# Kernel optimization log

Hardware: AMD Instinct MI355X
Metric: run time of the kernel (lower is better)

## Reference

```python
import jax, jax.numpy as jnp
import numpy as np

B, T, DF, S = 64, 16, 512, 196      # batch, ticks, backbone channels, tokens
D_IN, H = 512, 8                     # attention embed dim, heads
DH = D_IN // H
DM, MEM, HN = 1024, 25, 32           # d_model neurons, memory length, NLM hidden
NSA, NSO, DOUT = 512, 512, 512       # sync sizes (random-pairing), output dim


def _ln(x, g, b, eps=1e-5):
    m = x.mean(-1, keepdims=True)
    v = ((x - m) ** 2).mean(-1, keepdims=True)
    return (x - m) / jnp.sqrt(v + eps) * g + b


def setup_inputs() -> dict:
    key = jax.random.key(0)
    ks = jax.random.split(key, 24)
    rn = lambda k, sh, sc: jax.random.normal(k, sh, jnp.float32) * sc
    p = {}
    p['x'] = rn(ks[0], (B, T, DF, S), 1.0)
    # q_proj (LazyLinear: n_sync_action -> d_input)
    p['Wqp'] = rn(ks[1], (NSA, D_IN), (1.0 / NSA) ** 0.5); p['bqp'] = jnp.zeros((D_IN,))
    # kv_proj: LazyLinear(DF->D_IN) + LayerNorm
    p['Wkv'] = rn(ks[2], (DF, D_IN), (1.0 / DF) ** 0.5); p['bkv'] = jnp.zeros((D_IN,))
    p['g_kv'] = jnp.ones((D_IN,)); p['b_kv'] = jnp.zeros((D_IN,))
    # MultiheadAttention projections
    sc = (1.0 / D_IN) ** 0.5
    p['Wq'] = rn(ks[3], (D_IN, D_IN), sc); p['bq'] = jnp.zeros((D_IN,))
    p['Wk'] = rn(ks[4], (D_IN, D_IN), sc); p['bk'] = jnp.zeros((D_IN,))
    p['Wv'] = rn(ks[5], (D_IN, D_IN), sc); p['bv'] = jnp.zeros((D_IN,))
    p['Wo'] = rn(ks[6], (D_IN, D_IN), sc); p['bo'] = jnp.zeros((D_IN,))
    # synapses: Linear(D_IN+DM -> 2*DM) + GLU + LayerNorm(DM)
    p['Wsyn'] = rn(ks[7], (D_IN + DM, 2 * DM), (1.0 / (D_IN + DM)) ** 0.5)
    p['bsyn'] = jnp.zeros((2 * DM,))
    p['g_syn'] = jnp.ones((DM,)); p['b_syn'] = jnp.zeros((DM,))
    # NLM: per-neuron 2-layer MLP over memory window
    p['W1'] = rn(ks[8], (DM, MEM, HN), (1.0 / MEM) ** 0.5); p['b1'] = jnp.zeros((DM, HN))
    p['W2'] = rn(ks[9], (DM, HN), (1.0 / HN) ** 0.5); p['b2'] = jnp.zeros((DM,))
    # learned initial states
    p['init_act'] = rn(ks[10], (DM,), (1.0 / DM) ** 0.5)
    p['init_hist'] = rn(ks[11], (DM, MEM), (1.0 / (DM + MEM)) ** 0.5)
    # decay params (init zero in torch)
    p['decay_a'] = jnp.zeros((NSA,)); p['decay_o'] = jnp.zeros((NSO,))
    # output projection (LazyLinear: n_sync_out -> d_output)
    p['Wout'] = rn(ks[12], (NSO, DOUT), (1.0 / NSO) ** 0.5); p['bout'] = jnp.zeros((DOUT,))
    # random-pairing neuron indices (buffers, constants)
    p['li_a'] = jax.random.randint(ks[13], (NSA,), 0, DM, jnp.int32)
    p['ri_a'] = jax.random.randint(ks[14], (NSA,), 0, DM, jnp.int32)
    p['li_o'] = jax.random.randint(ks[15], (NSO,), 0, DM, jnp.int32)
    p['ri_o'] = jax.random.randint(ks[16], (NSO,), 0, DM, jnp.int32)
    return p


def reference(x, Wqp, bqp, Wkv, bkv, g_kv, b_kv, Wq, bq, Wk, bk, Wv, bv, Wo, bo,
              Wsyn, bsyn, g_syn, b_syn, W1, b1, W2, b2, init_act, init_hist,
              decay_a, decay_o, Wout, bout, li_a, ri_a, li_o, ri_o):
    r_a = jnp.exp(-jnp.clip(decay_a, 0.0, 15.0))   # [NSA]
    r_o = jnp.exp(-jnp.clip(decay_o, 0.0, 15.0))   # [NSO]
    act0 = jnp.broadcast_to(init_act, (B, DM))
    hist0 = jnp.broadcast_to(init_hist, (B, DM, MEM))
    # initial 'out' sync state (decay_alpha=pairwise, decay_beta=ones)
    ao0 = act0[:, li_o] * act0[:, ri_o]
    bo0 = jnp.ones_like(ao0)
    # 'action' state starts None -> zeros so first update gives alpha=pairwise, beta=1
    aa0 = jnp.zeros((B, NSA), x.dtype); ba0 = jnp.zeros((B, NSA), x.dtype)

    def mha(q, kv):
        # q [B,1,D_IN], kv [B,S,D_IN]
        qh = (q @ Wq + bq).reshape(B, 1, H, DH)
        kh = (kv @ Wk + bk).reshape(B, S, H, DH)
        vh = (kv @ Wv + bv).reshape(B, S, H, DH)
        sc = jnp.einsum('bqhd,bkhd->bhqk', qh, kh) / jnp.sqrt(jnp.float32(DH))
        a = jax.nn.softmax(sc, axis=-1)
        o = jnp.einsum('bhqk,bkhd->bqhd', a, vh).reshape(B, 1, D_IN)
        return o @ Wo + bo

    def tick(carry, xt):
        act, hist, aa, ba, ao, bo_ = carry
        # compute_kv: identity backbone, flatten(2).transpose(1,2) -> [B,S,DF]
        kv = _ln(jnp.swapaxes(xt, 1, 2) @ Wkv + bkv, g_kv, b_kv)
        # action sync
        aa = r_a * aa + act[:, li_a] * act[:, ri_a]
        ba = r_a * ba + 1.0
        sync_a = aa / jnp.sqrt(ba)
        q = (sync_a @ Wqp + bqp)[:, None, :]
        attn = mha(q, kv)[:, 0]                         # [B,D_IN]
        pre = jnp.concatenate([attn, act], axis=-1)     # [B,D_IN+DM]
        g = pre @ Wsyn + bsyn
        a_, b_ = jnp.split(g, 2, axis=-1)
        pre_act = _ln(a_ * jax.nn.sigmoid(b_), g_syn, b_syn)  # [B,DM]
        hist = jnp.concatenate([hist[:, :, 1:], pre_act[:, :, None]], axis=2)
        # NLM: per-neuron MLP over memory window
        h = jax.nn.relu(jnp.einsum('bnm,nmh->bnh', hist, W1) + b1)
        act = jnp.einsum('bnh,nh->bn', h, W2) + b2
        # out sync
        ao = r_o * ao + act[:, li_o] * act[:, ri_o]
        bo_ = r_o * bo_ + 1.0
        sync_o = ao / jnp.sqrt(bo_)
        pred = sync_o @ Wout + bout                      # [B,DOUT]
        logp = jax.nn.log_softmax(pred, axis=-1)
        ne = -(jnp.exp(logp) * logp).sum(-1) / jnp.log(jnp.float32(DOUT))
        cert = jnp.stack([ne, 1.0 - ne], axis=-1)        # [B,2]
        return (act, hist, aa, ba, ao, bo_), (pred, cert)

    xt = jnp.moveaxis(x, 1, 0)  # [T,B,DF,S]
    _, (preds, certs) = jax.lax.scan(tick, (act0, hist0, aa0, ba0, ao0, bo0), xt)
    predictions = jnp.moveaxis(preds, 0, -1)   # [B,DOUT,T]
    certainties = jnp.moveaxis(certs, 0, -1)   # [B,2,T]
    return predictions, certainties
```

## Files before the change

### kernel.cpp

```cpp
#include <hip/hip_runtime.h>
#include <stdint.h>
#include <stddef.h>

#define B_    64
#define T_    16
#define DF_   512
#define S_    196
#define DIN_  512
#define H_    8
#define DH_   64
#define DM_   1024
#define MEM_  25
#define HN_   32
#define MR_   (B_*S_)
#define TC_   2
#define NCH_  (T_/TC_)
#define MCC_  (MR_*TC_)

typedef short bf16x8 __attribute__((ext_vector_type(8)));
typedef short short4v __attribute__((ext_vector_type(4)));
typedef float f32x4  __attribute__((ext_vector_type(4)));

__device__ __forceinline__ float b2f(short h){
  unsigned u = ((unsigned)(unsigned short)h) << 16;
// ... 194 lines not shown
      __syncthreads();
      short* dst = xT + (size_t)((t0n2 + ti)*B_ + b) * S_ * DIN_;
      #pragma unroll
      for (int i = 0; i < 4; ++i) {
        int s  = s0 + ty + i*8;
        int df = df0 + tx;
        if (s < S_) dst[(size_t)s*DF_ + df] = f2b(tile[tx*33 + ty+i*8]);
      }
      __syncthreads();
    }
  } else if (op == 1) {
    int twin = tid >> 8;
    short* lA = (short*)pool;
    short* lB = (short*)(pool + 16384 + 16384*twin);
    int p = idx; if (p > 391) p = 391;
    int bx = p % 196, byp = p / 196;
    const short* xTn = xT + (size_t)t0n1 * MR_ * 512;
    gemm_body<0,0>(tid & 255, bx, byp*2 + twin, twin == 0, lA, lB,
                   xTn, WkvT, kvpN, bkv, bkv, 1 << 30,
                   nullptr, nullptr, nullptr, nullptr,
                   McN, 512, 512, 512, 512);
  } else if (op == 2) {
    int blk = idx;
    int w = tid >> 6, l = tid & 63;
    for (int i = 0; i < 8; ++i) {
      int r = blk*64 + i*8 + w;
      if (r < McN) {
        bf16x8 v8 = *(const bf16x8*)&kvpN[(size_t)r*512 + l*8];
        float s = 0.f, s2 = 0.f;
        #pragma unroll
        for (int j = 0; j < 8; ++j) { float v = b2f(v8[j]); s += v; s2 += v*v; }
        #pragma unroll
        for (int m = 1; m < 64; m <<= 1) { s += __shfl_xor(s, m, 64); s2 += __shfl_xor(s2, m, 64); }
        if (l == 0) {
          float mean = s * (1.f/512.f);
          float var  = s2 * (1.f/512.f) - mean*mean;
          muN[r] = mean;
          ivN[r] = rsqrtf(var + 1e-5f);
        }
      }
    }
  } else if (op == 3) {
    int twin = tid >> 8;
    short* lA = (short*)pool;
    short* lB = (short*)(pool + 16384 + 16384*twin);
    int p = idx; if (p > 783) p = 783;
    int bx = p % 8, byp = p / 8;
    gemm_body<0,2>(tid & 255, bx, byp*2 + twin, twin == 0, lA, lB,
                   WkkvT, kvpN, KVTN, nullptr, nullptr, 0,
                   muN, ivN, gw, bw, 1024, McN, 512, 512, McN);
  }
}

__device__ __forceinline__ void attn_body(int b, int tid, float* smem,
    const float* actT, float* aa, float* ba,
    const int* li_a, const int* ri_a, const float* decay_a,
    const short* WqqB, const float* bqh,
    const short* KVT, int ldkv, int ti, short* preb)
{
  float* syncL = smem;
  float* qhL   = smem + 512;
  float* pL    = smem + 1024;
  int j = tid;
  float rr = expf(-clip015(decay_a[j]));
  float prod = actT[li_a[j]*64 + b] * actT[ri_a[j]*64 + b];
  float a2 = rr*aa[b*512+j] + prod; aa[b*512+j] = a2;
  float bb2 = rr*ba[b*512+j] + 1.f;  ba[b*512+j] = bb2;
  syncL[j] = a2 * rsqrtf(bb2);
  __syncthreads();
  float qa = bqh[j];
  #pragma unroll 8
  for (int k = 0; k < 512; ++k) qa += syncL[k]*b2f(WqqB[k*512+j]);
  qhL[j] = qa;
  __syncthreads();
  int h = tid >> 6, l = tid & 63;
  const size_t cb = (size_t)(ti*B_ + b) * S_;
  const short* Kb = KVT + (size_t)(h*64)*ldkv + cb;
  int s3 = 192 + l; int s3c = s3 < S_ ? s3 : S_-1;
  float sc0=0.f, sc1=0.f, sc2=0.f, sc3=0.f;
  #pragma unroll 8
  for (int d = 0; d < 64; ++d) {
    const short* kr = Kb + (size_t)d*ldkv;
    float qv = qhL[h*64 + d];
    sc0 += qv * b2f(kr[l]);
    sc1 += qv * b2f(kr[64 + l]);
    sc2 += qv * b2f(kr[128 + l]);
    sc3 += qv * b2f(kr[s3c]);
  }
  sc0 *= 0.125f; sc1 *= 0.125f; sc2 *= 0.125f;
  sc3 = (s3 < S_) ? sc3*0.125f : -1e30f;
  float mx = fmaxf(fmaxf(sc0, sc1), fmaxf(sc2, sc3));
  #pragma unroll
  for (int k = 32; k >= 1; k >>= 1) mx = fmaxf(mx, __shfl_xor(mx, k, 64));
  float p0 = expf(sc0-mx), p1 = expf(sc1-mx), p2 = expf(sc2-mx), p3 = expf(sc3-mx);
  pL[h*256 + l] = p0; pL[h*256 + 64+l] = p1;
  pL[h*256 + 128+l] = p2; pL[h*256 + 192+l] = p3;
  float ps = p0+p1+p2+p3;
  #pragma unroll
  for (int k = 32; k >= 1; k >>= 1) ps += __shfl_xor(ps, k, 64);
  float inv = 1.f / ps;
  __syncthreads();
  const short4v* vrow = (const short4v*)(KVT + (size_t)(512 + h*64 + l)*ldkv + cb);
  const float* pp = pL + h*256;
  float ac0=0.f, ac1=0.f, ac2=0.f, ac3=0.f;
  #pragma unroll 7
  for (int c = 0; c < 49; ++c) {
    short4v v4 = vrow[c];
    ac0 += pp[c*4]   * b2f(v4.x);
    ac1 += pp[c*4+1] * b2f(v4.y);
    ac2 += pp[c*4+2] * b2f(v4.z);
    ac3 += pp[c*4+3] * b2f(v4.w);
  }
  float accv = (ac0+ac1)+(ac2+ac3);
  preb[(size_t)b*1536 + h*64 + l] = f2b(accv * inv);
}

__device__ __forceinline__ void outk_body(int tt, int b, int tid,
    float* syncL, float* wred,
    const float* actT, float* ao, float* bo_s,
    const int* li_o, const int* ri_o, const float* decay_o,
    const short* WoutB, const float* bout, float* out)
{
  int j = tid;
  float rr = expf(-clip015(decay_o[j]));
  float prod = actT[li_o[j]*64 + b] * actT[ri_o[j]*64 + b];
  float a2 = rr*ao[b*512+j] + prod; ao[b*512+j] = a2;
  float bb2 = rr*bo_s[b*512+j] + 1.f; bo_s[b*512+j] = bb2;
  syncL[j] = a2 * rsqrtf(bb2);
  __syncthreads();
  float a = bout[j];
  #pragma unroll 8
  for (int k = 0; k < 512; ++k) a += syncL[k]*b2f(WoutB[k*512+j]);
  out[((size_t)b*512 + j)*16 + tt] = a;
  int w = tid >> 6, l = tid & 63;
  float m = a;
  #pragma unroll
  for (int k = 32; k >= 1; k >>= 1) m = fmaxf(m, __shfl_xor(m, k, 64));
  if (l == 0) wred[w] = m;
  __syncthreads();
  float M = wred[0];
  #pragma unroll
  for (int k = 1; k < 8; ++k) M = fmaxf(M, wred[k]);
  float e = expf(a - M);
  float z = e, s1 = e*(a - M);
  #pragma unroll
  for (int k = 32; k >= 1; k >>= 1) { z += __shfl_xor(z, k, 64); s1 += __shfl_xor(s1, k, 64); }
  if (l == 0) { wred[8+w] = z; wred[16+w] = s1; }
  __syncthreads();
  if (tid == 0) {
    float Z = 0.f, S1 = 0.f;
    #pragma unroll
    for (int k = 0; k < 8; ++k) { Z += wred[8+k]; S1 += wred[16+k]; }
    float plp = S1 / Z - logf(Z);
    float ne = -plp * (1.f/logf(512.f));
    out[524288 + (size_t)b*32 + tt]      = ne;
    out[524288 + (size_t)b*32 + 16 + tt] = 1.f - ne;
  }
}

__device__ __forceinline__ void synglu_body(int bid, int tid, char* pool,
    const short* preb, const short* WsynP, const float* bsynF, float* u)
{
  f32x4* part = (f32x4*)pool;
  int w = tid >> 6, l = tid & 63;
  int mf = w & 3, kh = w >> 2;
  int arow = mf*16 + (l & 15);
  int kbase = kh*768 + (l >> 4)*8;
  const short* ap = preb + (size_t)arow*1536 + kbase;
  const short* bp = WsynP + (size_t)(bid*16 + (l & 15))*1536 + kbase;
  f32x4 acc = (f32x4){0.f,0.f,0.f,0.f};
  #pragma unroll 4
  for (int ks = 0; ks < 24; ++ks) {
    bf16x8 av = *(const bf16x8*)(ap + ks*32);
    bf16x8 bv = *(const bf16x8*)(bp + ks*32);
    acc = __builtin_amdgcn_mfma_f32_16x16x32_bf16(av, bv, acc, 0, 0, 0);
  }
  part[w*64 + l] = acc;
  __syncthreads();
  if (w < 4) {
    f32x4 o1 = part[w*64 + l], o2 = part[(w+4)*64 + l];
    int c = l & 15;
    int colg = bid*8 + (c & 7);
    float bias = (c < 8) ? bsynF[colg] : bsynF[1024 + colg];
    float tv[4], pv[4];
    #pragma unroll
    for (int r2 = 0; r2 < 4; ++r2) tv[r2] = o1[r2] + o2[r2] + bias;
    #pragma unroll
    for (int r2 = 0; r2 < 4; ++r2) pv[r2] = __shfl_xor(tv[r2], 8, 64);
    if (c < 8) {
      #pragma unroll
      for (int r2 = 0; r2 < 4; ++r2) {
        float uu = tv[r2] * (1.f/(1.f + expf(-pv[r2])));
        int brow = w*16 + (l >> 4)*4 + r2;
        u[brow*1024 + colg] = uu;
      }
    }
  }
}

__device__ __forceinline__ void nlmln_body(int bid, int tid, char* pool,
    const float* u, const float* gsyn, const float* bln, float* hist,
    const float* W1, const float* b1, const float* W2, const float* b2,
    float* actT, short* preb, int t)
{
  float* mstat = (float*)pool;
  float* istat = mstat + 64;
  {
    int b = tid >> 3, p = tid & 7;
    const float* up = u + b*1024 + p*128;
    float s = 0.f, s2 = 0.f;
    #pragma unroll 8
    for (int i = 0; i < 128; ++i) { float v = up[i]; s += v; s2 += v*v; }
    #pragma unroll
    for (int k = 4; k >= 1; k >>= 1) { s += __shfl_xor(s, k, 64); s2 += __shfl_xor(s2, k, 64); }
    if (p == 0) {
      float mean = s * (1.f/1024.f);
      float var  = s2 * (1.f/1024.f) - mean*mean;
      mstat[b] = mean;
      istat[b] = rsqrtf(var + 1e-5f);
    }
  }
  __syncthreads();
  int n = (bid << 3) + (tid >> 6), b = tid & 63;
  float nv = (u[b*1024 + n] - mstat[b]) * istat[b] * gsyn[n] + bln[n];
  int slot = t % MEM_;
  hist[((size_t)n*MEM_ + slot)*64 + b] = nv;
  float h[32];
  #pragma unroll
  for (int j = 0; j < 32; ++j) h[j] = b1[n*32+j];
  #pragma unroll 5
  for (int m = 0; m < MEM_; ++m) {
    int phys = (t + 1 + m) % MEM_;
    float hv = (m == MEM_-1) ? nv : hist[((size_t)n*MEM_ + phys)*64 + b];
    const float* wp = &W1[((size_t)n*MEM_ + m)*32];
    #pragma unroll
    for (int j = 0; j < 32; ++j) h[j] += hv * wp[j];
  }
  float acc = b2[n];
  #pragma unroll
  for (int j = 0; j < 32; ++j) acc += fmaxf(h[j], 0.f) * W2[n*32+j];
  actT[n*64 + b] = acc;
  preb[(size_t)b*1536 + 512 + n] = f2b(acc);
}

#define PIGGY_ARGS int opA, int pfA, int nA, int opB, int pfB, \
    const float* __restrict__ xg, int t0n1, int t0n2, short* __restrict__ xTg, \
    const short* __restrict__ WkvT, \
    const float* __restrict__ bkv, short* __restrict__ kvpN, \
    float* __restrict__ muN, float* __restrict__ ivN, \
    const short* __restrict__ WkkvT, const float* __restrict__ gw, \
    const float* __restrict__ bw, short* __restrict__ KVTN, int McN
#define PIGGY_CALL do { \
    int pb = (int)blockIdx.x - 128; \
    int op_, idx_; \
    if (pb < nA) { op_ = opA; idx_ = pfA + pb; } \
    else         { op_ = opB; idx_ = pfB + (pb - nA); } \
    run_piggy(tid, op_, idx_, pool, xg, t0n1, t0n2, xTg, WkvT, bkv, \
              kvpN, muN, ivN, WkkvT, gw, bw, KVTN, McN); \
  } while (0)

__global__ __launch_bounds__(512) void stageA(
    const float* __restrict__ actT,
    float* __restrict__ aa, float* __restrict__ ba,
    const int* __restrict__ li_a, const int* __restrict__ ri_a,
    const float* __restrict__ decay_a,
    const short* __restrict__ WqqB, const float* __restrict__ bqh,
    const short* __restrict__ KVT, int ldkv, int ti,
    short* __restrict__ preb,
    float* __restrict__ ao, float* __restrict__ bo_s,
    const int* __restrict__ li_o, const int* __restrict__ ri_o,
    const float* __restrict__ decay_o,
    const short* __restrict__ WoutB, const float* __restrict__ bout,
    float* __restrict__ out, int t, PIGGY_ARGS)
{
  __shared__ __attribute__((aligned(16))) char pool[49152];
  const int bid = blockIdx.x, tid = threadIdx.x;
  if (bid < 128) {
    float* smem = (float*)pool;
    if (bid < 64)
      attn_body(bid, tid, smem, actT, aa, ba, li_a, ri_a, decay_a,
                WqqB, bqh, KVT, ldkv, ti, preb);
    else if (t > 0)
      outk_body(t-1, bid-64, tid, smem, smem+512, actT, ao, bo_s,
                li_o, ri_o, decay_o, WoutB, bout, out);
  } else {
    PIGGY_CALL;
  }
}

__global__ __launch_bounds__(512) void stageB(
    const short* __restrict__ preb, const short* __restrict__ WsynP,
    const float* __restrict__ bsynF, float* __restrict__ u, PIGGY_ARGS)
{
  __shared__ __attribute__((aligned(16))) char pool[49152];
  const int bid = blockIdx.x, tid = threadIdx.x;
  if (bid < 128) synglu_body(bid, tid, pool, preb, WsynP, bsynF, u);
  else PIGGY_CALL;
}

__global__ __launch_bounds__(512) void stageC(
    const float* __restrict__ u, const float* __restrict__ gsyn,
    const float* __restrict__ bln, float* __restrict__ hist,
    const float* __restrict__ W1, const float* __restrict__ b1,
    const float* __restrict__ W2, const float* __restrict__ b2,
    float* __restrict__ actT, short* __restrict__ preb, int t, PIGGY_ARGS)
{
  __shared__ __attribute__((aligned(16))) char pool[49152];
  const int bid = blockIdx.x, tid = threadIdx.x;
  if (bid < 128) nlmln_body(bid, tid, pool, u, gsyn, bln, hist,
                            W1, b1, W2, b2, actT, preb, t);
  else PIGGY_CALL;
}

__global__ __launch_bounds__(512) void outk_fin(
    const float* __restrict__ actT,
    float* __restrict__ ao, float* __restrict__ bo_s,
    const int* __restrict__ li_o, const int* __restrict__ ri_o,
    const float* __restrict__ decay_o,
    const short* __restrict__ WoutB, const float* __restrict__ bout,
    float* __restrict__ out)
{
  __shared__ __attribute__((aligned(16))) float smem[544];
  outk_body(T_-1, blockIdx.x, threadIdx.x, smem, smem+512, actT, ao, bo_s,
            li_o, ri_o, decay_o, WoutB, bout, out);
}

__global__ __launch_bounds__(256) void xpose_x(const float* __restrict__ x,
                                               short* __restrict__ xT, int t0, int tc)
{
  __shared__ float tile[32][33];
  int df0 = blockIdx.x*32, s0 = blockIdx.y*32;
  int z = blockIdx.z;
  int b = z / tc, ti = z % tc;
  int tx = threadIdx.x & 31, ty = threadIdx.x >> 5;
  const float* src = x + (size_t)(b*T_ + t0 + ti) * DF_ * S_;
  #pragma unroll
  for (int i = 0; i < 4; ++i) {
    int df = df0 + ty + i*8;
    int s  = s0 + tx;
    tile[ty+i*8][tx] = (s < S_) ? src[(size_t)df*S_ + s] : 0.f;
  }
  __syncthreads();
  short* dst = xT + (size_t)((t0 + ti)*B_ + b) * S_ * DIN_;
  #pragma unroll
  for (int i = 0; i < 4; ++i) {
    int s  = s0 + ty + i*8;
    int df = df0 + tx;
    if (s < S_) dst[(size_t)s*DF_ + df] = f2b(tile[tx][ty+i*8]);
  }
}

__global__ __launch_bounds__(256) void ln_stats(const short* __restrict__ in,
    float* __restrict__ mu, float* __restrict__ iv, int nrows)
{
  int w = threadIdx.x >> 6, l = threadIdx.x & 63;
  int r = blockIdx.x*4 + w;
  if (r >= nrows) return;
  bf16x8 v8 = *(const bf16x8*)&in[(size_t)r*512 + l*8];
  float s = 0.f, s2 = 0.f;
  #pragma unroll
  for (int j = 0; j < 8; ++j) { float v = b2f(v8[j]); s += v; s2 += v*v; }
  #pragma unroll
  for (int m = 1; m < 64; m <<= 1) { s += __shfl_xor(s, m, 64); s2 += __shfl_xor(s2, m, 64); }
  if (l == 0) {
    float mean = s * (1.f/512.f);
    float var  = s2 * (1.f/512.f) - mean*mean;
    mu[r] = mean;
    iv[r] = rsqrtf(var + 1e-5f);
  }
}

__global__ __launch_bounds__(256) void prep_all(
    const float* __restrict__ Wkv, const float* __restrict__ Wk,
    const float* __restrict__ Wv,  const float* __restrict__ Wsyn,
    const float* __restrict__ Wq,  const float* __restrict__ Wqp,
    const float* __restrict__ Wo,  const float* __restrict__ Wout,
    const float* __restrict__ g_kv, const float* __restrict__ b_kv,
    const float* __restrict__ bk, const float* __restrict__ bv,
    const float* __restrict__ bqp, const float* __restrict__ bq,
    const float* __restrict__ bo_p, const float* __restrict__ bsyn,
    short* __restrict__ WkvT, short* __restrict__ WkkvT,
    short* __restrict__ WsynF, short* __restrict__ WsynTt,
    short* __restrict__ WqT, short* __restrict__ WqpB,
    short* __restrict__ WoB, short* __restrict__ WoutB,
    float* __restrict__ bqh, float* __restrict__ bsynF,
    float* __restrict__ gw, float* __restrict__ bw,
    float* __restrict__ aa, float* __restrict__ ba,
    float* __restrict__ ao, float* __restrict__ bo_s,
    float* __restrict__ actT, float* __restrict__ hist,
    short* __restrict__ preb,
    const float* __restrict__ init_act, const float* __restrict__ init_hist,
    const int* __restrict__ li_o, const int* __restrict__ ri_o,
    const float* __restrict__ x, short* __restrict__ xT)
{
  __shared__ float tile[32][33];
  const int blk = blockIdx.x, tid = threadIdx.x;
  auto wtr = [&](const float* in, short* out, int bx, int by,
                 int C, int ldo, int coff, const float* scale){
    int c0 = bx*32, r0 = by*32;
    int tx = tid & 31, ty = tid >> 5;
    #pragma unroll
    for (int i = 0; i < 4; ++i) {
      int r = r0+ty+i*8;
      float sc = scale ? scale[r] : 1.f;
      tile[ty+i*8][tx] = in[(size_t)r*C + c0+tx] * sc;
    }
    __syncthreads();
    #pragma unroll
    for (int i = 0; i < 4; ++i)
      out[(size_t)(c0+ty+i*8)*ldo + coff + r0+tx] = f2b(tile[tx][ty+i*8]);
  };
  auto cvt4 = [&](const float* in, short* out, int sb){
    int i = (sb*256 + tid)*4;
    #pragma unroll
    for (int j = 0; j < 4; ++j) out[i+j] = f2b(in[i+j]);
  };
  auto bfold = [&](const float* vec, const float* W, const float* base,
                   float* out, int n, int ldw){
    float a = base ? base[n] : 0.f;
    #pragma unroll 8
    for (int k = 0; k < 512; ++k) a += vec[k]*W[(size_t)k*ldw + n];
    out[n] = a;
  };

  if (blk < 256)       wtr(Wkv, WkvT, blk & 15, blk >> 4, 512, 512, 0, nullptr);
  else if (blk < 512)  { int s = blk-256;  wtr(Wk, WkkvT, s & 15, s >> 4, 512, 512, 0, g_kv); }
  else if (blk < 768)  { int s = blk-512;  wtr(Wv, WkkvT + (size_t)512*512, s & 15, s >> 4, 512, 512, 0, g_kv); }
  else if (blk < 2816) { int s = blk-768;  wtr(Wsyn + (size_t)512*2048, WsynF, s % 64, s / 64, 2048, 1536, 512, nullptr); }
  else if (blk < 3840) { int s = blk-2816; wtr(Wsyn, WsynTt, s % 64, s / 64, 2048, 512, 0, nullptr); }
  else if (blk < 4096) { int s = blk-3840; wtr(Wq, WqT, s & 15, s >> 4, 512, 512, 0, nullptr); }
  else if (blk < 4352) cvt4(Wqp,  WqpB,  blk-4096);
  else if (blk < 4608) cvt4(Wo,   WoB,   blk-4352);
  else if (blk < 4864) cvt4(Wout, WoutB, blk-4608);
  else if (blk < 4882) {
    int j = blk-4864;
    if (j < 2)        bfold(bqp,  Wq,   bq,   bqh,   j*256 + tid,      512);
    else if (j < 10)  bfold(bo_p, Wsyn, bsyn, bsynF, (j-2)*256 + tid,  2048);
    else if (j < 12)  bfold(g_kv, Wk,   nullptr, gw,       (j-10)*256 + tid, 512);
    else if (j < 14)  bfold(g_kv, Wv,   nullptr, gw + 512, (j-12)*256 + tid, 512);
    else if (j < 16)  bfold(b_kv, Wk,   bk,   bw,       (j-14)*256 + tid, 512);
    else              bfold(b_kv, Wv,   bv,   bw + 512, (j-16)*256 + tid, 512);
  } else if (blk < 11282) {
    int i = (blk-4882)*256 + tid;
    if (i < 64*512) {
      aa[i] = 0.f; ba[i] = 0.f;
      int j = i & 511;
      ao[i] = init_act[li_o[j]] * init_act[ri_o[j]];
      bo_s[i] = 1.f;
    }
    if (i < 65536) {
      int n = i >> 6, b = i & 63;
      actT[i] = init_act[n];
      preb[(size_t)b*1536 + 512 + n] = f2b(init_act[n]);
    }
    if (i < DM_*MEM_*64) {
      int nm = i >> 6;
      hist[i] = init_hist[nm];
    }
  } else {
    int tx = tid & 31, ty = tid >> 5;
    int base = (blk - 11282) * 16;
    for (int it = 0; it < 16; ++it) {
      int gt = base + it;
      int df0 = (gt & 15) * 32;
      int r = gt >> 4;
      int s0 = (r % 7) * 32;
      int z = r / 7;
      int b = z >> 2, t = z & 3;
      const float* src = x + (size_t)(b*T_ + t) * DF_ * S_;
      #pragma unroll
      for (int i = 0; i < 4; ++i) {
        int df = df0 + ty + i*8;
        int s  = s0 + tx;
        tile[ty+i*8][tx] = (s < S_) ? src[(size_t)df*S_ + s] : 0.f;
      }
      __syncthreads();
      short* dst = xT + (size_t)(t*B_ + b) * S_ * DIN_;
      #pragma unroll
      for (int i = 0; i < 4; ++i) {
        int s  = s0 + ty + i*8;
        int df = df0 + tx;
        if (s < S_) dst[(size_t)s*DF_ + df] = f2b(tile[tx][ty+i*8]);
      }
      __syncthreads();
    }
  }
}

extern "C" void kernel_launch(void* const* d_in, const int* in_sizes, int n_in,
                              void* d_out, int out_size, void* d_ws, size_t ws_size,
                              hipStream_t stream)
{
  (void)in_sizes; (void)n_in; (void)out_size;
  const float* x       = (const float*)d_in[0];
  const float* Wqp     = (const float*)d_in[1];
  const float* bqp     = (const float*)d_in[2];
  const float* Wkv     = (const float*)d_in[3];
  const float* bkv     = (const float*)d_in[4];
  const float* g_kv    = (const float*)d_in[5];
  const float* b_kv    = (const float*)d_in[6];
  const float* Wq      = (const float*)d_in[7];
  const float* bq      = (const float*)d_in[8];
  const float* Wk      = (const float*)d_in[9];
  const float* bk      = (const float*)d_in[10];
  const float* Wv      = (const float*)d_in[11];
  const float* bv      = (const float*)d_in[12];
  const float* Wo      = (const float*)d_in[13];
  const float* bo_p    = (const float*)d_in[14];
  const float* Wsyn    = (const float*)d_in[15];
  const float* bsyn    = (const float*)d_in[16];
  const float* g_syn   = (const float*)d_in[17];
  const float* b_syn   = (const float*)d_in[18];
  const float* W1      = (const float*)d_in[19];
  const float* b1      = (const float*)d_in[20];
  const float* W2      = (const float*)d_in[21];
  const float* b2      = (const float*)d_in[22];
  const float* init_act  = (const float*)d_in[23];
  const float* init_hist = (const float*)d_in[24];
  const float* decay_a = (const float*)d_in[25];
  const float* decay_o = (const float*)d_in[26];
  const float* Wout    = (const float*)d_in[27];
  const float* bout    = (const float*)d_in[28];
  const int* li_a = (const int*)d_in[29];
  const int* ri_a = (const int*)d_in[30];
  const int* li_o = (const int*)d_in[31];
  const int* ri_o = (const int*)d_in[32];

  char* ws = (char*)d_ws;
  size_t off = 0;
  auto alloc = [&](size_t bytes) { char* p = ws + off; off += (bytes + 255) & ~(size_t)255; return p; };
  short* WkvT   = (short*)alloc(512*512*2);
  short* WkkvT  = (short*)alloc(1024*512*2);
  short* WsynF  = (short*)alloc(2048*1536*2);
  short* WsynP  = (short*)alloc(2048*1536*2);
  short* WsynTt = (short*)alloc(2048*512*2);
  short* WqpB   = (short*)alloc(512*512*2);
  short* WqT    = (short*)alloc(512*512*2);
  short* WoB    = (short*)alloc(512*512*2);
  short* WqqB   = (short*)alloc(512*512*2);
  short* WoutB  = (short*)alloc(512*512*2);
  float* bqh    = (float*)alloc(512*4);
  float* bsynF  = (float*)alloc(2048*4);
  float* gw     = (float*)alloc(1024*4);
  float* bw     = (float*)alloc(1024*4);
  short* preb   = (short*)alloc(64*1536*2);
  float* u      = (float*)alloc(64*1024*4);
  float* aa     = (float*)alloc(64*512*4);
  float* ba     = (float*)alloc(64*512*4);
  float* ao     = (float*)alloc(64*512*4);
  float* bo_s   = (float*)alloc(64*512*4);
  float* actT   = (float*)alloc(1024*64*4);
  float* hist   = (float*)alloc((size_t)1024*25*64*4);
  size_t fixed_end = off;

  const size_t szXT  = (size_t)T_*MR_*512*2;
  const size_t szKVP = (size_t)MCC_*512*2;
  const size_t szKVT = (size_t)MCC_*1024*2;
  const size_t szST  = (size_t)MCC_*4;
  size_t need_full = fixed_end + szXT + 2*szKVP + 2*szKVT + 4*szST + 4096;
  bool pig_en = (ws_size >= need_full);

  short* xT = (short*)alloc(szXT);
  short* kvpB[2]; short* KVTB[2]; float* muB[2]; float* ivB[2];
  kvpB[0] = (short*)alloc(szKVP);
  KVTB[0] = (short*)alloc(szKVT);
  muB[0]  = (float*)alloc(szST);
  ivB[0]  = (float*)alloc(szST);
  if (pig_en) {
    kvpB[1] = (short*)alloc(szKVP);
    KVTB[1] = (short*)alloc(szKVT);
    muB[1]  = (float*)alloc(szST);
    ivB[1]  = (float*)alloc(szST);
  } else {
    kvpB[1] = kvpB[0]; KVTB[1] = KVTB[0]; muB[1] = muB[0]; ivB[1] = ivB[0];
  }

  const int BIG = 1 << 30;
  const float* FN = nullptr;

  prep_all<<<13074, 256, 0, stream>>>(Wkv, Wk, Wv, Wsyn, Wq, Wqp, Wo, Wout,
      g_kv, b_kv, bk, bv, bqp, bq, bo_p, bsyn,
      WkvT, WkkvT, WsynF, WsynTt, WqT, WqpB, WoB, WoutB,
      bqh, bsynF, gw, bw, aa, ba, ao, bo_s, actT, hist, preb,
      init_act, init_hist, li_o, ri_o, x, xT);
  if (!pig_en)
    xpose_x<<<dim3(16,7,B_*(T_-2*TC_)), 256, 0, stream>>>(x, xT, 2*TC_, T_-2*TC_);
  gemm_prep3<<<864, 256, 0, stream>>>(WqpB, WqT, WqqB, WsynTt, WoB, WsynF,
                                      xT, WkvT, bkv, kvpB[0]);
  permstats<<<2048 + MCC_/4, 256, 0, stream>>>(WsynF, WsynP, kvpB[0], muB[0], ivB[0]);
  gemm_k<0,2><<<dim3(8,196), 256, 0, stream>>>(WkkvT, kvpB[0], KVTB[0], nullptr, nullptr, BIG,
                                               muB[0], ivB[0], gw, bw, 1024, MCC_, 512, 512, MCC_);

  auto run_pipe = [&](int c, short* kvpP, float* muP, float* ivP, short* KVTP){
    const short* xTc = xT + (size_t)c*TC_*MR_*512;
    gemm_k<0,0><<<dim3(196,4), 256, 0, stream>>>(xTc, WkvT, kvpP, bkv, bkv, BIG,
                                                 FN, FN, FN, FN, MCC_, 512, 512, 512, 512);
    ln_stats<<<MCC_/4, 256, 0, stream>>>(kvpP, muP, ivP, MCC_);
    gemm_k<0,2><<<dim3(8,196), 256, 0, stream>>>(WkkvT, kvpP, KVTP, nullptr, nullptr, BIG,
                                                 muP, ivP, gw, bw, 1024, MCC_, 512, 512, MCC_);
  };

  auto pigcfg = [](int q, bool p123, bool p4,
                   int& opA, int& pfA, int& nA, int& opB, int& pfB, int& nB){
    opA = 0; pfA = 0; nA = 0; opB = 0; pfB = 0; nB = 0;
    if (q == 0 || q == 1) {
      if (p123) { opA = 1; pfA = q*196; nA = 196; }
      if (p4)   { opB = 4; pfB = q*224; nB = 224; }
    } else if (q == 2) {
      if (p123) { opA = 2; pfA = 0; nA = 392; }
    } else {
      if (p123) { opA = 3; pfA = (q-3)*262; nA = (q == 5) ? 260 : 262; }
    }
  };

  for (int c = 0; c < NCH_; ++c) {
    int par = pig_en ? (c & 1) : 0;
    int nxt = pig_en ? (par ^ 1) : 0;
    if (!pig_en && c > 0) run_pipe(c, kvpB[0], muB[0], ivB[0], KVTB[0]);
    bool p123 = pig_en && (c < NCH_-1);
    bool p4   = pig_en && (c < NCH_-2);
    int t0n1 = (c < NCH_-1) ? (c+1)*TC_ : 0;
    int t0n2 = (c < NCH_-2) ? (c+2)*TC_ : 0;
    for (int ti = 0; ti < TC_; ++ti) {
      int t = c*TC_ + ti;
      int oA, fA, nA, oB, fB, nB;
      pigcfg(ti*3+0, p123, p4, oA, fA, nA, oB, fB, nB);
      stageA<<<128+nA+nB, 512, 0, stream>>>(actT, aa, ba, li_a, ri_a, decay_a,
          WqqB, bqh, KVTB[par], MCC_, ti, preb,
          ao, bo_s, li_o, ri_o, decay_o, WoutB, bout, (float*)d_out, t,
          oA, fA, nA, oB, fB, x, t0n1, t0n2, xT, WkvT, bkv,
          kvpB[nxt], muB[nxt], ivB[nxt], WkkvT, gw, bw, KVTB[nxt], MCC_);
      pigcfg(ti*3+1, p123, p4, oA, fA, nA, oB, fB, nB);
      stageB<<<128+nA+nB, 512, 0, stream>>>(preb, WsynP, bsynF, u,
          oA, fA, nA, oB, fB, x, t0n1, t0n2, xT, WkvT, bkv,
          kvpB[nxt], muB[nxt], ivB[nxt], WkkvT, gw, bw, KVTB[nxt], MCC_);
      pigcfg(ti*3+2, p123, p4, oA, fA, nA, oB, fB, nB);
      stageC<<<128+nA+nB, 512, 0, stream>>>(u, g_syn, b_syn, hist,
          W1, b1, W2, b2, actT, preb, t,
          oA, fA, nA, oB, fB, x, t0n1, t0n2, xT, WkvT, bkv,
          kvpB[nxt], muB[nxt], ivB[nxt], WkkvT, gw, bw, KVTB[nxt], MCC_);
    }
  }
  outk_fin<<<64, 512, 0, stream>>>(actT, ao, bo_s, li_o, ri_o, decay_o,
                                   WoutB, bout, (float*)d_out);
}
```

Before: 2.046 ms.

## Fuse NLM/LayerNorm, output sync and attention into one per-batch stage kernel

Merges the per-tick stageC (LayerNorm + NLM), the output-sync head and stageA (action sync + attention) into a single stageCA kernel where each of 64 blocks handles one batch row. The block keeps activations in shared memory, which removes one launch per tick and the global actT round trip. The history buffer is relaid out batch-major so each block owns its own slice, and the piggybacked KV-precompute work is redistributed across two launches instead of three. In exchange, this phase now uses only 64 blocks that each do the full 1024-neuron NLM serially with two neurons per thread, which reduces parallelism on the critical path.

```diff
diff --git a/kernel.cpp b/kernel.cpp
--- a/kernel.cpp
+++ b/kernel.cpp
@@ -270,197 +270,6 @@
   }
 }
 
-__device__ __forceinline__ void attn_body(int b, int tid, float* smem,
-    const float* actT, float* aa, float* ba,
-    const int* li_a, const int* ri_a, const float* decay_a,
-    const short* WqqB, const float* bqh,
-    const short* KVT, int ldkv, int ti, short* preb)
-{
-  float* syncL = smem;
-  float* qhL   = smem + 512;
-  float* pL    = smem + 1024;
-  int j = tid;
-  float rr = expf(-clip015(decay_a[j]));
-  float prod = actT[li_a[j]*64 + b] * actT[ri_a[j]*64 + b];
-  float a2 = rr*aa[b*512+j] + prod; aa[b*512+j] = a2;
-  float bb2 = rr*ba[b*512+j] + 1.f;  ba[b*512+j] = bb2;
-  syncL[j] = a2 * rsqrtf(bb2);
-  __syncthreads();
-  float qa = bqh[j];
-  #pragma unroll 8
-  for (int k = 0; k < 512; ++k) qa += syncL[k]*b2f(WqqB[k*512+j]);
-  qhL[j] = qa;
-  __syncthreads();
-  int h = tid >> 6, l = tid & 63;
-  const size_t cb = (size_t)(ti*B_ + b) * S_;
-  const short* Kb = KVT + (size_t)(h*64)*ldkv + cb;
-  int s3 = 192 + l; int s3c = s3 < S_ ? s3 : S_-1;
-  float sc0=0.f, sc1=0.f, sc2=0.f, sc3=0.f;
-  #pragma unroll 8
-  for (int d = 0; d < 64; ++d) {
-    const short* kr = Kb + (size_t)d*ldkv;
-    float qv = qhL[h*64 + d];
-    sc0 += qv * b2f(kr[l]);
-    sc1 += qv * b2f(kr[64 + l]);
-    sc2 += qv * b2f(kr[128 + l]);
-    sc3 += qv * b2f(kr[s3c]);
-  }
-  sc0 *= 0.125f; sc1 *= 0.125f; sc2 *= 0.125f;
-  sc3 = (s3 < S_) ? sc3*0.125f : -1e30f;
-  float mx = fmaxf(fmaxf(sc0, sc1), fmaxf(sc2, sc3));
-  #pragma unroll
-  for (int k = 32; k >= 1; k >>= 1) mx = fmaxf(mx, __shfl_xor(mx, k, 64));
-  float p0 = expf(sc0-mx), p1 = expf(sc1-mx), p2 = expf(sc2-mx), p3 = expf(sc3-mx);
-  pL[h*256 + l] = p0; pL[h*256 + 64+l] = p1;
-  pL[h*256 + 128+l] = p2; pL[h*256 + 192+l] = p3;
-  float ps = p0+p1+p2+p3;
-  #pragma unroll
-  for (int k = 32; k >= 1; k >>= 1) ps += __shfl_xor(ps, k, 64);
-  float inv = 1.f / ps;
-  __syncthreads();
-  const short4v* vrow = (const short4v*)(KVT + (size_t)(512 + h*64 + l)*ldkv + cb);
-  const float* pp = pL + h*256;
-  float ac0=0.f, ac1=0.f, ac2=0.f, ac3=0.f;
-  #pragma unroll 7
-  for (int c = 0; c < 49; ++c) {
-    short4v v4 = vrow[c];
-    ac0 += pp[c*4]   * b2f(v4.x);
-    ac1 += pp[c*4+1] * b2f(v4.y);
-    ac2 += pp[c*4+2] * b2f(v4.z);
-    ac3 += pp[c*4+3] * b2f(v4.w);
-  }
-  float accv = (ac0+ac1)+(ac2+ac3);
-  preb[(size_t)b*1536 + h*64 + l] = f2b(accv * inv);
-}
-
-__device__ __forceinline__ void outk_body(int tt, int b, int tid,
-    float* syncL, float* wred,
-    const float* actT, float* ao, float* bo_s,
-    const int* li_o, const int* ri_o, const float* decay_o,
-    const short* WoutB, const float* bout, float* out)
-{
-  int j = tid;
-  float rr = expf(-clip015(decay_o[j]));
-  float prod = actT[li_o[j]*64 + b] * actT[ri_o[j]*64 + b];
-  float a2 = rr*ao[b*512+j] + prod; ao[b*512+j] = a2;
-  float bb2 = rr*bo_s[b*512+j] + 1.f; bo_s[b*512+j] = bb2;
-  syncL[j] = a2 * rsqrtf(bb2);
-  __syncthreads();
-  float a = bout[j];
-  #pragma unroll 8
-  for (int k = 0; k < 512; ++k) a += syncL[k]*b2f(WoutB[k*512+j]);
-  out[((size_t)b*512 + j)*16 + tt] = a;
-  int w = tid >> 6, l = tid & 63;
-  float m = a;
-  #pragma unroll
-  for (int k = 32; k >= 1; k >>= 1) m = fmaxf(m, __shfl_xor(m, k, 64));
-  if (l == 0) wred[w] = m;
-  __syncthreads();
-  float M = wred[0];
-  #pragma unroll
-  for (int k = 1; k < 8; ++k) M = fmaxf(M, wred[k]);
-  float e = expf(a - M);
-  float z = e, s1 = e*(a - M);
-  #pragma unroll
-  for (int k = 32; k >= 1; k >>= 1) { z += __shfl_xor(z, k, 64); s1 += __shfl_xor(s1, k, 64); }
-  if (l == 0) { wred[8+w] = z; wred[16+w] = s1; }
-  __syncthreads();
-  if (tid == 0) {
-    float Z = 0.f, S1 = 0.f;
-    #pragma unroll
-    for (int k = 0; k < 8; ++k) { Z += wred[8+k]; S1 += wred[16+k]; }
-    float plp = S1 / Z - logf(Z);
-    float ne = -plp * (1.f/logf(512.f));
-    out[524288 + (size_t)b*32 + tt]      = ne;
-    out[524288 + (size_t)b*32 + 16 + tt] = 1.f - ne;
-  }
-}
-
-__device__ __forceinline__ void synglu_body(int bid, int tid, char* pool,
-    const short* preb, const short* WsynP, const float* bsynF, float* u)
-{
-  f32x4* part = (f32x4*)pool;
-  int w = tid >> 6, l = tid & 63;
-  int mf = w & 3, kh = w >> 2;
-  int arow = mf*16 + (l & 15);
-  int kbase = kh*768 + (l >> 4)*8;
-  const short* ap = preb + (size_t)arow*1536 + kbase;
-  const short* bp = WsynP + (size_t)(bid*16 + (l & 15))*1536 + kbase;
-  f32x4 acc = (f32x4){0.f,0.f,0.f,0.f};
-  #pragma unroll 4
-  for (int ks = 0; ks < 24; ++ks) {
-    bf16x8 av = *(const bf16x8*)(ap + ks*32);
-    bf16x8 bv = *(const bf16x8*)(bp + ks*32);
-    acc = __builtin_amdgcn_mfma_f32_16x16x32_bf16(av, bv, acc, 0, 0, 0);
-  }
-  part[w*64 + l] = acc;
-  __syncthreads();
-  if (w < 4) {
-    f32x4 o1 = part[w*64 + l], o2 = part[(w+4)*64 + l];
-    int c = l & 15;
-    int colg = bid*8 + (c & 7);
-    float bias = (c < 8) ? bsynF[colg] : bsynF[1024 + colg];
-    float tv[4], pv[4];
-    #pragma unroll
-    for (int r2 = 0; r2 < 4; ++r2) tv[r2] = o1[r2] + o2[r2] + bias;
-    #pragma unroll
-    for (int r2 = 0; r2 < 4; ++r2) pv[r2] = __shfl_xor(tv[r2], 8, 64);
-    if (c < 8) {
-      #pragma unroll
-      for (int r2 = 0; r2 < 4; ++r2) {
-        float uu = tv[r2] * (1.f/(1.f + expf(-pv[r2])));
-        int brow = w*16 + (l >> 4)*4 + r2;
-        u[brow*1024 + colg] = uu;
-      }
-    }
-  }
-}
-
-__device__ __forceinline__ void nlmln_body(int bid, int tid, char* pool,
-    const float* u, const float* gsyn, const float* bln, float* hist,
-    const float* W1, const float* b1, const float* W2, const float* b2,
-    float* actT, short* preb, int t)
-{
-  float* mstat = (float*)pool;
-  float* istat = mstat + 64;
-  {
-    int b = tid >> 3, p = tid & 7;
-    const float* up = u + b*1024 + p*128;
-    float s = 0.f, s2 = 0.f;
-    #pragma unroll 8
-    for (int i = 0; i < 128; ++i) { float v = up[i]; s += v; s2 += v*v; }
-    #pragma unroll
-    for (int k = 4; k >= 1; k >>= 1) { s += __shfl_xor(s, k, 64); s2 += __shfl_xor(s2, k, 64); }
-    if (p == 0) {
-      float mean = s * (1.f/1024.f);
-      float var  = s2 * (1.f/1024.f) - mean*mean;
-      mstat[b] = mean;
-      istat[b] = rsqrtf(var + 1e-5f);
-    }
-  }
-  __syncthreads();
-  int n = (bid << 3) + (tid >> 6), b = tid & 63;
-  float nv = (u[b*1024 + n] - mstat[b]) * istat[b] * gsyn[n] + bln[n];
-  int slot = t % MEM_;
-  hist[((size_t)n*MEM_ + slot)*64 + b] = nv;
-  float h[32];
-  #pragma unroll
-  for (int j = 0; j < 32; ++j) h[j] = b1[n*32+j];
-  #pragma unroll 5
-  for (int m = 0; m < MEM_; ++m) {
-    int phys = (t + 1 + m) % MEM_;
-    float hv = (m == MEM_-1) ? nv : hist[((size_t)n*MEM_ + phys)*64 + b];
-    const float* wp = &W1[((size_t)n*MEM_ + m)*32];
-    #pragma unroll
-    for (int j = 0; j < 32; ++j) h[j] += hv * wp[j];
-  }
-  float acc = b2[n];
-  #pragma unroll
-  for (int j = 0; j < 32; ++j) acc += fmaxf(h[j], 0.f) * W2[n*32+j];
-  actT[n*64 + b] = acc;
-  preb[(size_t)b*1536 + 512 + n] = f2b(acc);
-}
-
 #define PIGGY_ARGS int opA, int pfA, int nA, int opB, int pfB, \
     const float* __restrict__ xg, int t0n1, int t0n2, short* __restrict__ xTg, \
     const short* __restrict__ WkvT, \
@@ -468,8 +277,8 @@
     float* __restrict__ muN, float* __restrict__ ivN, \
     const short* __restrict__ WkkvT, const float* __restrict__ gw, \
     const float* __restrict__ bw, short* __restrict__ KVTN, int McN
-#define PIGGY_CALL do { \
-    int pb = (int)blockIdx.x - 128; \
+#define PIGGY_BODY(BASE) do { \
+    int pb = (int)blockIdx.x - (BASE); \
     int op_, idx_; \
     if (pb < nA) { op_ = opA; idx_ = pfA + pb; } \
     else         { op_ = opB; idx_ = pfB + (pb - nA); } \
@@ -477,8 +286,13 @@
               kvpN, muN, ivN, WkkvT, gw, bw, KVTN, McN); \
   } while (0)
 
-__global__ __launch_bounds__(512) void stageA(
-    const float* __restrict__ actT,
+__global__ __launch_bounds__(512) void stageCA(
+    const float* __restrict__ u,
+    const float* __restrict__ gsyn, const float* __restrict__ bln,
+    float* __restrict__ histB,
+    const float* __restrict__ W1, const float* __restrict__ b1,
+    const float* __restrict__ W2, const float* __restrict__ b2,
+    const float* __restrict__ init_act,
     float* __restrict__ aa, float* __restrict__ ba,
     const int* __restrict__ li_a, const int* __restrict__ ri_a,
     const float* __restrict__ decay_a,
@@ -489,58 +303,222 @@
     const int* __restrict__ li_o, const int* __restrict__ ri_o,
     const float* __restrict__ decay_o,
     const short* __restrict__ WoutB, const float* __restrict__ bout,
-    float* __restrict__ out, int t, PIGGY_ARGS)
+    float* __restrict__ out, int t, int dopre, int doattn, PIGGY_ARGS)
+{
+  __shared__ __attribute__((aligned(16))) char pool[49152];
+  const int bid = blockIdx.x, tid = threadIdx.x;
+  if (bid < 64) {
+    const int b = bid;
+    float* actL  = (float*)pool;
+    float* syncL = actL + 1024;
+    float* wred  = syncL + 512;
+    float* qhL   = wred + 32;
+    float* pL    = qhL + 512;
+    int w = tid >> 6, l = tid & 63;
+    if (dopre) {
+      const int tp = t - 1;
+      const int slot = tp % MEM_;
+      float v0 = u[b*1024 + tid], v1 = u[b*1024 + 512 + tid];
+      float s = v0 + v1, s2 = v0*v0 + v1*v1;
+      #pragma unroll
+      for (int k = 32; k >= 1; k >>= 1) { s += __shfl_xor(s, k, 64); s2 += __shfl_xor(s2, k, 64); }
+      if (l == 0) { wred[w] = s; wred[8+w] = s2; }
+      __syncthreads();
+      float S = 0.f, S2 = 0.f;
+      #pragma unroll
+      for (int k = 0; k < 8; ++k) { S += wred[k]; S2 += wred[8+k]; }
+      float mean = S * (1.f/1024.f);
+      float var  = S2 * (1.f/1024.f) - mean*mean;
+      float inv  = rsqrtf(var + 1e-5f);
+      float nv0 = (v0 - mean)*inv*gsyn[tid]     + bln[tid];
+      float nv1 = (v1 - mean)*inv*gsyn[tid+512] + bln[tid+512];
+      float h[32];
+      {
+        const int n = tid;
+        float* hb = histB + ((size_t)b*1024 + n)*MEM_;
+        #pragma unroll
+        for (int j = 0; j < 32; ++j) h[j] = b1[n*32+j];
+        #pragma unroll 5
+        for (int m = 0; m < MEM_; ++m) {
+          int phys = (tp + 1 + m) % MEM_;
+          float hv = (m == MEM_-1) ? nv0 : hb[phys];
+          const float* wp = &W1[((size_t)n*MEM_ + m)*32];
+          #pragma unroll
+          for (int j = 0; j < 32; ++j) h[j] += hv * wp[j];
+        }
+        hb[slot] = nv0;
+        float acc = b2[n];
+        #pragma unroll
+        for (int j = 0; j < 32; ++j) acc += fmaxf(h[j], 0.f) * W2[n*32+j];
+        actL[n] = acc;
+        preb[(size_t)b*1536 + 512 + n] = f2b(acc);
+      }
+      {
+        const int n = tid + 512;
+        float* hb = histB + ((size_t)b*1024 + n)*MEM_;
+        #pragma unroll
+        for (int j = 0; j < 32; ++j) h[j] = b1[n*32+j];
+        #pragma unroll 5
+        for (int m = 0; m < MEM_; ++m) {
+          int phys = (tp + 1 + m) % MEM_;
+          float hv = (m == MEM_-1) ? nv1 : hb[phys];
+          const float* wp = &W1[((size_t)n*MEM_ + m)*32];
+          #pragma unroll
+          for (int j = 0; j < 32; ++j) h[j] += hv * wp[j];
+        }
+        hb[slot] = nv1;
+        float acc = b2[n];
+        #pragma unroll
+        for (int j = 0; j < 32; ++j) acc += fmaxf(h[j], 0.f) * W2[n*32+j];
+        actL[n] = acc;
+        preb[(size_t)b*1536 + 512 + n] = f2b(acc);
+      }
+      __syncthreads();
+      {
+        int j = tid;
+        float rr = expf(-clip015(decay_o[j]));
+        float prod = actL[li_o[j]] * actL[ri_o[j]];
+        float a2 = rr*ao[b*512+j] + prod; ao[b*512+j] = a2;
+        float bb2 = rr*bo_s[b*512+j] + 1.f; bo_s[b*512+j] = bb2;
+        syncL[j] = a2 * rsqrtf(bb2);
+        __syncthreads();
+        float a = bout[j];
+        #pragma unroll 8
+        for (int k = 0; k < 512; ++k) a += syncL[k]*b2f(WoutB[k*512+j]);
+        out[((size_t)b*512 + j)*16 + tp] = a;
+        float m = a;
+        #pragma unroll
+        for (int k = 32; k >= 1; k >>= 1) m = fmaxf(m, __shfl_xor(m, k, 64));
+        if (l == 0) wred[w] = m;
+        __syncthreads();
+        float M = wred[0];
+        #pragma unroll
+        for (int k = 1; k < 8; ++k) M = fmaxf(M, wred[k]);
+        float e = expf(a - M);
+        float z = e, s1 = e*(a - M);
+        #pragma unroll
+        for (int k = 32; k >= 1; k >>= 1) { z += __shfl_xor(z, k, 64); s1 += __shfl_xor(s1, k, 64); }
+        if (l == 0) { wred[8+w] = z; wred[16+w] = s1; }
+        __syncthreads();
+        if (tid == 0) {
+          float Z = 0.f, S1 = 0.f;
+          #pragma unroll
+          for (int k = 0; k < 8; ++k) { Z += wred[8+k]; S1 += wred[16+k]; }
+          float plp = S1 / Z - logf(Z);
+          float ne = -plp * (1.f/logf(512.f));
+          out[524288 + (size_t)b*32 + tp]      = ne;
+          out[524288 + (size_t)b*32 + 16 + tp] = 1.f - ne;
+        }
+      }
+    } else {
+      actL[tid]       = init_act[tid];
+      actL[tid + 512] = init_act[tid + 512];
+    }
+    __syncthreads();
+    if (doattn) {
+      int j = tid;
+      float rr = expf(-clip015(decay_a[j]));
+      float prod = actL[li_a[j]] * actL[ri_a[j]];
+      float a2 = rr*aa[b*512+j] + prod; aa[b*512+j] = a2;
+      float bb2 = rr*ba[b*512+j] + 1.f;  ba[b*512+j] = bb2;
+      syncL[j] = a2 * rsqrtf(bb2);
+      __syncthreads();
+      float qa = bqh[j];
+      #pragma unroll 8
+      for (int k = 0; k < 512; ++k) qa += syncL[k]*b2f(WqqB[k*512+j]);
+      qhL[j] = qa;
+      __syncthreads();
+      int h8 = tid >> 6;
+      const size_t cb = (size_t)(ti*B_ + b) * S_;
+      const short* Kb = KVT + (size_t)(h8*64)*ldkv + cb;
+      int s3 = 192 + l; int s3c = s3 < S_ ? s3 : S_-1;
+      float sc0=0.f, sc1=0.f, sc2=0.f, sc3=0.f;
+      #pragma unroll 8
+      for (int d = 0; d < 64; ++d) {
+        const short* kr = Kb + (size_t)d*ldkv;
+        float qv = qhL[h8*64 + d];
+        sc0 += qv * b2f(kr[l]);
+        sc1 += qv * b2f(kr[64 + l]);
+        sc2 += qv * b2f(kr[128 + l]);
+        sc3 += qv * b2f(kr[s3c]);
+      }
+      sc0 *= 0.125f; sc1 *= 0.125f; sc2 *= 0.125f;
+      sc3 = (s3 < S_) ? sc3*0.125f : -1e30f;
+      float mx = fmaxf(fmaxf(sc0, sc1), fmaxf(sc2, sc3));
+      #pragma unroll
+      for (int k = 32; k >= 1; k >>= 1) mx = fmaxf(mx, __shfl_xor(mx, k, 64));
+      float p0 = expf(sc0-mx), p1 = expf(sc1-mx), p2 = expf(sc2-mx), p3 = expf(sc3-mx);
+      pL[h8*256 + l] = p0; pL[h8*256 + 64+l] = p1;
+      pL[h8*256 + 128+l] = p2; pL[h8*256 + 192+l] = p3;
+      float ps = p0+p1+p2+p3;
+      #pragma unroll
+      for (int k = 32; k >= 1; k >>= 1) ps += __shfl_xor(ps, k, 64);
+      float inv2 = 1.f / ps;
+      __syncthreads();
+      const short4v* vrow = (const short4v*)(KVT + (size_t)(512 + h8*64 + l)*ldkv + cb);
+      const float* pp = pL + h8*256;
+      float ac0=0.f, ac1=0.f, ac2=0.f, ac3=0.f;
+      #pragma unroll 7
+      for (int c = 0; c < 49; ++c) {
+        short4v v4 = vrow[c];
+        ac0 += pp[c*4]   * b2f(v4.x);
+        ac1 += pp[c*4+1] * b2f(v4.y);
+        ac2 += pp[c*4+2] * b2f(v4.z);
+        ac3 += pp[c*4+3] * b2f(v4.w);
+      }
+      float accv = (ac0+ac1)+(ac2+ac3);
+      preb[(size_t)b*1536 + h8*64 + l] = f2b(accv * inv2);
+    }
+  } else {
+    PIGGY_BODY(64);
+  }
+}
+
+__global__ __launch_bounds__(512) void stageB(
+    const short* __restrict__ preb, const short* __restrict__ WsynP,
+    const float* __restrict__ bsynF, float* __restrict__ u, PIGGY_ARGS)
 {
   __shared__ __attribute__((aligned(16))) char pool[49152];
   const int bid = blockIdx.x, tid = threadIdx.x;
   if (bid < 128) {
-    float* smem = (float*)pool;
-    if (bid < 64)
-      attn_body(bid, tid, smem, actT, aa, ba, li_a, ri_a, decay_a,
-                WqqB, bqh, KVT, ldkv, ti, preb);
-    else if (t > 0)
-      outk_body(t-1, bid-64, tid, smem, smem+512, actT, ao, bo_s,
-                li_o, ri_o, decay_o, WoutB, bout, out);
+    f32x4* part = (f32x4*)pool;
+    int w = tid >> 6, l = tid & 63;
+    int mf = w & 3, kh = w >> 2;
+    int arow = mf*16 + (l & 15);
+    int kbase = kh*768 + (l >> 4)*8;
+    const short* ap = preb + (size_t)arow*1536 + kbase;
+    const short* bp = WsynP + (size_t)(bid*16 + (l & 15))*1536 + kbase;
+    f32x4 acc = (f32x4){0.f,0.f,0.f,0.f};
+    #pragma unroll 4
+    for (int ks = 0; ks < 24; ++ks) {
+      bf16x8 av = *(const bf16x8*)(ap + ks*32);
+      bf16x8 bv = *(const bf16x8*)(bp + ks*32);
+      acc = __builtin_amdgcn_mfma_f32_16x16x32_bf16(av, bv, acc, 0, 0, 0);
+    }
+    part[w*64 + l] = acc;
+    __syncthreads();
+    if (w < 4) {
+      f32x4 o1 = part[w*64 + l], o2 = part[(w+4)*64 + l];
+      int c = l & 15;
+      int colg = bid*8 + (c & 7);
+      float bias = (c < 8) ? bsynF[colg] : bsynF[1024 + colg];
+      float tv[4], pv[4];
+      #pragma unroll
+      for (int r2 = 0; r2 < 4; ++r2) tv[r2] = o1[r2] + o2[r2] + bias;
+      #pragma unroll
+      for (int r2 = 0; r2 < 4; ++r2) pv[r2] = __shfl_xor(tv[r2], 8, 64);
+      if (c < 8) {
+        #pragma unroll
+        for (int r2 = 0; r2 < 4; ++r2) {
+          float uu = tv[r2] * (1.f/(1.f + expf(-pv[r2])));
+          int brow = w*16 + (l >> 4)*4 + r2;
+          u[brow*1024 + colg] = uu;
+        }
+      }
+    }
   } else {
-    PIGGY_CALL;
-  }
-}
-
-__global__ __launch_bounds__(512) void stageB(
-    const short* __restrict__ preb, const short* __restrict__ WsynP,
-    const float* __restrict__ bsynF, float* __restrict__ u, PIGGY_ARGS)
-{
-  __shared__ __attribute__((aligned(16))) char pool[49152];
-  const int bid = blockIdx.x, tid = threadIdx.x;
-  if (bid < 128) synglu_body(bid, tid, pool, preb, WsynP, bsynF, u);
-  else PIGGY_CALL;
-}
-
-__global__ __launch_bounds__(512) void stageC(
-    const float* __restrict__ u, const float* __restrict__ gsyn,
-    const float* __restrict__ bln, float* __restrict__ hist,
-    const float* __restrict__ W1, const float* __restrict__ b1,
-    const float* __restrict__ W2, const float* __restrict__ b2,
-    float* __restrict__ actT, short* __restrict__ preb, int t, PIGGY_ARGS)
-{
-  __shared__ __attribute__((aligned(16))) char pool[49152];
-  const int bid = blockIdx.x, tid = threadIdx.x;
-  if (bid < 128) nlmln_body(bid, tid, pool, u, gsyn, bln, hist,
-                            W1, b1, W2, b2, actT, preb, t);
-  else PIGGY_CALL;
-}
-
-__global__ __launch_bounds__(512) void outk_fin(
-    const float* __restrict__ actT,
-    float* __restrict__ ao, float* __restrict__ bo_s,
-    const int* __restrict__ li_o, const int* __restrict__ ri_o,
-    const float* __restrict__ decay_o,
-    const short* __restrict__ WoutB, const float* __restrict__ bout,
-    float* __restrict__ out)
-{
-  __shared__ __attribute__((aligned(16))) float smem[544];
-  outk_body(T_-1, blockIdx.x, threadIdx.x, smem, smem+512, actT, ao, bo_s,
-            li_o, ri_o, decay_o, WoutB, bout, out);
+    PIGGY_BODY(128);
+  }
 }
 
 __global__ __launch_bounds__(256) void xpose_x(const float* __restrict__ x,
@@ -605,8 +583,7 @@
     float* __restrict__ gw, float* __restrict__ bw,
     float* __restrict__ aa, float* __restrict__ ba,
     float* __restrict__ ao, float* __restrict__ bo_s,
-    float* __restrict__ actT, float* __restrict__ hist,
-    short* __restrict__ preb,
+    float* __restrict__ histB, short* __restrict__ preb,
     const float* __restrict__ init_act, const float* __restrict__ init_hist,
     const int* __restrict__ li_o, const int* __restrict__ ri_o,
     const float* __restrict__ x, short* __restrict__ xT)
@@ -668,12 +645,10 @@
     }
     if (i < 65536) {
       int n = i >> 6, b = i & 63;
-      actT[i] = init_act[n];
       preb[(size_t)b*1536 + 512 + n] = f2b(init_act[n]);
     }
     if (i < DM_*MEM_*64) {
-      int nm = i >> 6;
-      hist[i] = init_hist[nm];
+      histB[i] = init_hist[i % 25600];
     }
   } else {
     int tx = tid & 31, ty = tid >> 5;
@@ -767,8 +742,7 @@
   float* ba     = (float*)alloc(64*512*4);
   float* ao     = (float*)alloc(64*512*4);
   float* bo_s   = (float*)alloc(64*512*4);
-  float* actT   = (float*)alloc(1024*64*4);
-  float* hist   = (float*)alloc((size_t)1024*25*64*4);
+  float* histB  = (float*)alloc((size_t)64*1024*25*4);
   size_t fixed_end = off;
 
   const size_t szXT  = (size_t)T_*MR_*512*2;
@@ -799,7 +773,7 @@
   prep_all<<<13074, 256, 0, stream>>>(Wkv, Wk, Wv, Wsyn, Wq, Wqp, Wo, Wout,
       g_kv, b_kv, bk, bv, bqp, bq, bo_p, bsyn,
       WkvT, WkkvT, WsynF, WsynTt, WqT, WqpB, WoB, WoutB,
-      bqh, bsynF, gw, bw, aa, ba, ao, bo_s, actT, hist, preb,
+      bqh, bsynF, gw, bw, aa, ba, ao, bo_s, histB, preb,
       init_act, init_hist, li_o, ri_o, x, xT);
   if (!pig_en)
     xpose_x<<<dim3(16,7,B_*(T_-2*TC_)), 256, 0, stream>>>(x, xT, 2*TC_, T_-2*TC_);
@@ -821,14 +795,12 @@
   auto pigcfg = [](int q, bool p123, bool p4,
                    int& opA, int& pfA, int& nA, int& opB, int& pfB, int& nB){
     opA = 0; pfA = 0; nA = 0; opB = 0; pfB = 0; nB = 0;
-    if (q == 0 || q == 1) {
-      if (p123) { opA = 1; pfA = q*196; nA = 196; }
-      if (p4)   { opB = 4; pfB = q*224; nB = 224; }
-    } else if (q == 2) {
-      if (p123) { opA = 2; pfA = 0; nA = 392; }
-    } else {
-      if (p123) { opA = 3; pfA = (q-3)*262; nA = (q == 5) ? 260 : 262; }
-    }
+    if (q == 0)      { if (p123) { opA = 1; pfA = 0;   nA = 392; } }
+    else if (q == 1) { if (p123) { opA = 2; pfA = 0;   nA = 392; }
+                       if (p4)   { opB = 4; pfB = 0;   nB = 224; } }
+    else if (q == 2) { if (p123) { opA = 3; pfA = 0;   nA = 392; }
+                       if (p4)   { opB = 4; pfB = 224; nB = 224; } }
+    else             { if (p123) { opA = 3; pfA = 392; nA = 392; } }
   };
 
   for (int c = 0; c < NCH_; ++c) {
@@ -842,23 +814,25 @@
     for (int ti = 0; ti < TC_; ++ti) {
       int t = c*TC_ + ti;
       int oA, fA, nA, oB, fB, nB;
-      pigcfg(ti*3+0, p123, p4, oA, fA, nA, oB, fB, nB);
-      stageA<<<128+nA+nB, 512, 0, stream>>>(actT, aa, ba, li_a, ri_a, decay_a,
-          WqqB, bqh, KVTB[par], MCC_, ti, preb,
-          ao, bo_s, li_o, ri_o, decay_o, WoutB, bout, (float*)d_out, t,
+      pigcfg(ti*2+0, p123, p4, oA, fA, nA, oB, fB, nB);
+      stageCA<<<64+nA+nB, 512, 0, stream>>>(u, g_syn, b_syn, histB,
+          W1, b1, W2, b2, init_act,
+          aa, ba, li_a, ri_a, decay_a, WqqB, bqh, KVTB[par], MCC_, ti, preb,
+          ao, bo_s, li_o, ri_o, decay_o, WoutB, bout, (float*)d_out,
+          t, (t > 0) ? 1 : 0, 1,
           oA, fA, nA, oB, fB, x, t0n1, t0n2, xT, WkvT, bkv,
           kvpB[nxt], muB[nxt], ivB[nxt], WkkvT, gw, bw, KVTB[nxt], MCC_);
-      pigcfg(ti*3+1, p123, p4, oA, fA, nA, oB, fB, nB);
+      pigcfg(ti*2+1, p123, p4, oA, fA, nA, oB, fB, nB);
       stageB<<<128+nA+nB, 512, 0, stream>>>(preb, WsynP, bsynF, u,
           oA, fA, nA, oB, fB, x, t0n1, t0n2, xT, WkvT, bkv,
           kvpB[nxt], muB[nxt], ivB[nxt], WkkvT, gw, bw, KVTB[nxt], MCC_);
-      pigcfg(ti*3+2, p123, p4, oA, fA, nA, oB, fB, nB);
-      stageC<<<128+nA+nB, 512, 0, stream>>>(u, g_syn, b_syn, hist,
-          W1, b1, W2, b2, actT, preb, t,
-          oA, fA, nA, oB, fB, x, t0n1, t0n2, xT, WkvT, bkv,
-          kvpB[nxt], muB[nxt], ivB[nxt], WkkvT, gw, bw, KVTB[nxt], MCC_);
-    }
-  }
-  outk_fin<<<64, 512, 0, stream>>>(actT, ao, bo_s, li_o, ri_o, decay_o,
-                                   WoutB, bout, (float*)d_out);
-}
+    }
+  }
+  stageCA<<<64, 512, 0, stream>>>(u, g_syn, b_syn, histB,
+      W1, b1, W2, b2, init_act,
+      aa, ba, li_a, ri_a, decay_a, WqqB, bqh, KVTB[(NCH_-1)&1], MCC_, 1, preb,
+      ao, bo_s, li_o, ri_o, decay_o, WoutB, bout, (float*)d_out,
+      T_, 1, 0,
+      0, 0, 0, 0, 0, x, 0, 0, xT, WkvT, bkv,
+      kvpB[0], muB[0], ivB[0], WkkvT, gw, bw, KVTB[0], MCC_);
+}
```

New measurement: 3.251 ms. 58.9% more time.
